# Optimization experiments

Hardware: AMD Instinct MI355X
Metric: run time of the kernel (lower is better)

Reference implementation:

```python
import jax, jax.numpy as jnp
import numpy as np

D = 768      # embedding_dim
M = 3072     # mlp_dim
G = 4        # num_expert_groups
E = 8        # experts_per_group
KG = 2       # k_groups
KE = 4       # k_experts
EPS = 1e-6   # gate weight threshold from the torch module


def setup_inputs() -> dict:
    key = jax.random.key(0)
    ks = jax.random.split(key, 9)
    x = jax.random.normal(ks[0], (1, 1024, D), dtype=jnp.float32)
    Wg = jax.random.normal(ks[1], (D, G), dtype=jnp.float32) * 0.02
    bg = jax.random.normal(ks[2], (G,), dtype=jnp.float32) * 0.01
    We = jax.random.normal(ks[3], (G, D, E), dtype=jnp.float32) * 0.02
    be = jax.random.normal(ks[4], (G, E), dtype=jnp.float32) * 0.01
    W1 = jax.random.normal(ks[5], (G, E, D, M), dtype=jnp.float32) * 0.02
    b1 = jax.random.normal(ks[6], (G, E, M), dtype=jnp.float32) * 0.01
    W2 = jax.random.normal(ks[7], (G, E, M, D), dtype=jnp.float32) * 0.02
    b2 = jax.random.normal(ks[8], (G, E, D), dtype=jnp.float32) * 0.01
    return {"x": x, "Wg": Wg, "bg": bg, "We": We, "be": be,
            "W1": W1, "b1": b1, "W2": W2, "b2": b2}


def _topk_gates(logits, k):
    # top-k logits -> softmax over the k entries, then zero out weights < 1e-6
    top, idx = jax.lax.top_k(logits, k)
    gates = jax.nn.softmax(top, axis=-1)
    gates = jnp.where(gates >= EPS, gates, jnp.zeros_like(gates))
    return gates, idx


def reference(x, Wg, bg, We, be, W1, b1, W2, b2):
    orig_shape = x.shape
    xf = x.reshape(-1, D)  # [N, D]

    # ---- level 1: group gating (eval mode: clean logits, no noise) ----
    glog = xf @ Wg + bg                      # [N, G]
    ggates, gidx = _topk_gates(glog, KG)     # [N, KG]
    gw = jnp.einsum('nk,nkg->ng', ggates,
                    jax.nn.one_hot(gidx, G, dtype=xf.dtype))  # dense [N, G]

    # ---- level 2: expert gating within each group ----
    # computed densely for all groups; unselected groups get zero group weight
    elog = jnp.einsum('nd,gde->nge', xf, We) + be  # [N, G, E]
    egates, eidx = _topk_gates(elog, KE)            # [N, G, KE]
    ew = jnp.einsum('ngk,ngke->nge', egates,
                    jax.nn.one_hot(eidx, E, dtype=xf.dtype))  # dense [N, G, E]

    combine = gw[:, :, None] * ew  # [N, G, E] combine weights

    # ---- expert MLPs (dense compute, combine-weighted sum) ----
    y = jnp.zeros_like(xf)
    for g in range(G):  # small fixed loop over expert groups
        h = jax.nn.gelu(jnp.einsum('nd,edm->enm', xf, W1[g]) + b1[g][:, None, :],
                        approximate=False)               # [E, N, M]
        o = jnp.einsum('enm,emd->end', h, W2[g]) + b2[g][:, None, :]  # [E, N, D]
        y = y + jnp.einsum('end,ne->nd', o, combine[:, g, :])
    return y.reshape(orig_shape)
```

## Files before the change

### kernel.cpp

```cpp
#include <hip/hip_runtime.h>
#include <hip/hip_bf16.h>
#include <math.h>

#define NTOK 1024
#define DDIM 768
#define MDIM 3072
#define GN 4
#define EN 8
#define NEXP 32
#define NPAIR 8192
#define EPSW 1e-6f
#define BYSPAN 3

typedef __attribute__((ext_vector_type(4))) float f32x4;
typedef __attribute__((ext_vector_type(4))) int   i32x4;
typedef __attribute__((ext_vector_type(4))) unsigned short u16x4;
typedef __attribute__((ext_vector_type(8))) __bf16 bf16x8;

__device__ __forceinline__ unsigned short f2bf(float f) {
  unsigned u = __builtin_bit_cast(unsigned, f);
  u += 0x7FFFu + ((u >> 16) & 1u);
  return (unsigned short)(u >> 16);
}

__global__ void init_kernel(int* __restrict__ p) { p[threadIdx.x] = 0; }

__global__ __launch_bounds__(256) void zero_y(float* __restrict__ y) {
  ((f32x4*)y)[blockIdx.x * 256 + threadIdx.x] = (f32x4){0.f, 0.f, 0.f, 0.f};
}

__global__ __launch_bounds__(256) void x2bf(const float* __restrict__ x,
                                            unsigned short* __restrict__ xb) {
  const int i = (blockIdx.x * 256 + threadIdx.x) * 16;
#pragma unroll
  for (int j = 0; j < 4; ++j) {
    const f32x4 v = *(const f32x4*)(x + i + j * 4);
    u16x4 p = { f2bf(v.x), f2bf(v.y), f2bf(v.z), f2bf(v.w) };
    *(u16x4*)(xb + i + j * 4) = p;
  }
}

__global__ __launch_bounds__(256) void gating_kernel(
    const float* __restrict__ x, const float* __restrict__ Wg,
    const float* __restrict__ bg, const float* __restrict__ We,
    const float* __restrict__ be, int* __restrict__ counts,
    int* __restrict__ pair_e, float* __restrict__ pair_w)
{
  __shared__ float xr[DDIM];
  __shared__ float logits[36];
  const int n = blockIdx.x;
  const int tid = threadIdx.x;
  const float* xp = x + (size_t)n * DDIM;
  for (int d = tid; d < DDIM; d += 256) xr[d] = xp[d];
  __syncthreads();

  const int w = tid >> 6, lane = tid & 63;
  for (int j = 0; j < 9; ++j) {
    const int o = w + 4 * j;
    float s = 0.f;
    if (o < 4) {
      for (int d = lane; d < DDIM; d += 64) s += xr[d] * Wg[d * GN + o];
    } else {
      const int g = (o - 4) >> 3, e = (o - 4) & 7;
      const float* wp = We + (size_t)g * DDIM * EN + e;
      for (int d = lane; d < DDIM; d += 64) s += xr[d] * wp[d * EN];
    }
    for (int off = 32; off; off >>= 1) s += __shfl_xor(s, off);
    if (lane == 0) logits[o] = s + ((o < 4) ? bg[o] : be[o - 4]);
  }
  __syncthreads();

  if (tid == 0) {
    float gl[4];
    for (int i = 0; i < 4; ++i) gl[i] = logits[i];
    int i0 = 0;
    for (int i = 1; i < 4; ++i) if (gl[i] > gl[i0]) i0 = i;
    int i1 = -1;
    for (int i = 0; i < 4; ++i) {
      if (i == i0) continue;
      if (i1 < 0 || gl[i] > gl[i1]) i1 = i;
    }
    const float m = gl[i0];
    const float e1 = expf(gl[i1] - m);
    const float s2 = 1.f + e1;
    float gv[2] = { 1.f / s2, e1 / s2 };
    int gi[2] = { i0, i1 };
    for (int r = 0; r < 2; ++r) if (gv[r] < EPSW) gv[r] = 0.f;

    for (int r = 0; r < 2; ++r) {
      const int g = gi[r];
      float el[8];
      for (int e = 0; e < 8; ++e) el[e] = logits[4 + g * 8 + e];
      int sel[4];
      for (int q = 0; q < 4; ++q) {
        int best = -1;
        for (int e = 0; e < 8; ++e) {
          bool used = false;
          for (int p = 0; p < q; ++p) if (sel[p] == e) used = true;
          if (used) continue;
          if (best < 0 || el[e] > el[best]) best = e;
        }
        sel[q] = best;
      }
      const float mm = el[sel[0]];
      float ex[4]; float ss = 0.f;
      for (int q = 0; q < 4; ++q) { ex[q] = expf(el[sel[q]] - mm); ss += ex[q]; }
      for (int q = 0; q < 4; ++q) {
        float ew = ex[q] / ss;
        if (ew < EPSW) ew = 0.f;
        const int gbl = g * 8 + sel[q];
        const int j = r * 4 + q;
        pair_e[n * 8 + j] = gbl;
        pair_w[n * 8 + j] = gv[r] * ew;
        atomicAdd(&counts[gbl], 1);
      }
    }
  }
}

__global__ void scan_kernel(const int* __restrict__ counts, int* __restrict__ offsets)
{
  if (threadIdx.x == 0) {
    int a = 0;
    for (int i = 0; i < NEXP; ++i) { offsets[i] = a; a += counts[i]; }
  }
}

__global__ __launch_bounds__(256) void scatter_kernel(
    const int* __restrict__ pair_e, const float* __restrict__ pair_w,
    const int* __restrict__ offsets, int* __restrict__ cursor,
    int* __restrict__ slot_tok, float* __restrict__ slot_w)
{
  const int idx = blockIdx.x * 256 + threadIdx.x;
  if (idx < NPAIR) {
    const int e = pair_e[idx];
    const int s = offsets[e] + atomicAdd(&cursor[e], 1);
    slot_tok[s] = idx >> 3;
    slot_w[s] = pair_w[idx];
  }
}

template<int K, int NLD, int EPI, int GATHER>
__global__ __launch_bounds__(256, 2) void moe_gemm_rs(
    const unsigned short* __restrict__ Abase, const float* __restrict__ W,
    const float* __restrict__ bias, const int* __restrict__ counts,
    const int* __restrict__ offsets, const float* __restrict__ slot_w,
    const int* __restrict__ slot_tok, unsigned short* __restrict__ Hout,
    float* __restrict__ Yout)
{
  constexpr int NT = K / 32;
  constexpr int BUFB = 16384;

  const int ge = blockIdx.z;
  const int cnt = counts[ge];
  const int nb = blockIdx.y;
  const int off = offsets[ge];
  const int tid = threadIdx.x;

  __shared__ __align__(16) unsigned char lds[2 * BUFB];

  const int am = tid >> 2, ac = tid & 3;
  const int asw0 = am * 64 + ((ac ^ ((am ^ (am >> 2)) & 3)) * 16);
  const int asw1 = asw0 + 4096;

  const int kq = tid >> 5, ln = tid & 31;
  const float* bp = W + (size_t)ge * K * NLD + (size_t)(kq * 4) * NLD + nb * 128 + ln;
  int bwr[4];
#pragma unroll
  for (int ii = 0; ii < 4; ++ii) {
    const int n = ln + 32 * ii;
    const int s = (n ^ (n >> 2)) & 3;
    bwr[ii] = 8192 + n * 64 + (((kq >> 1) ^ s) * 16) + ((kq & 1) * 8);
  }

  const int w = tid >> 6, lane = tid & 63;
  const int wr = (w >> 1) * 64, wc = (w & 1) * 64;
  const int l15 = lane & 15, l4 = lane >> 4;
  int aoff[4], boff[4];
#pragma unroll
  for (int mf = 0; mf < 4; ++mf) {
    const int m = wr + mf * 16 + l15;
    aoff[mf] = m * 64 + ((l4 ^ ((m ^ (m >> 2)) & 3)) * 16);
  }
#pragma unroll
  for (int nf = 0; nf < 4; ++nf) {
    const int n = wc + nf * 16 + l15;
    boff[nf] = 8192 + n * 64 + ((l4 ^ ((n ^ (n >> 2)) & 3)) * 16);
  }

  for (int by = blockIdx.x; by * 128 < cnt; by += BYSPAN) {
    int gr0 = by * 128 + am;      if (gr0 >= cnt) gr0 = cnt - 1;
    int gr1 = by * 128 + am + 64; if (gr1 >= cnt) gr1 = cnt - 1;
    const unsigned short* ap0;
    const unsigned short* ap1;
    if (GATHER) {
      ap0 = Abase + (size_t)slot_tok[off + gr0] * K + ac * 8;
      ap1 = Abase + (size_t)slot_tok[off + gr1] * K + ac * 8;
    } else {
      ap0 = Abase + (size_t)(off + gr0) * K + ac * 8;
      ap1 = Abase + (size_t)(off + gr1) * K + ac * 8;
    }

    f32x4 acc[4][4];
#pragma unroll
    for (int mf = 0; mf < 4; ++mf)
#pragma unroll
      for (int nf = 0; nf < 4; ++nf)
        acc[mf][nf] = (f32x4){0.f, 0.f, 0.f, 0.f};

    i32x4 aA0, aA1, aB0, aB1, aC0, aC1;
    float bA[16], bB[16], bC[16];

#define LOADA(T, R0, R1) { \
    R0 = *(const i32x4*)(ap0 + (T) * 32); \
    R1 = *(const i32x4*)(ap1 + (T) * 32); }
#define LOADB(T, BS) { _Pragma("unroll") \
    for (int ii = 0; ii < 4; ++ii) { _Pragma("unroll") \
      for (int jj = 0; jj < 4; ++jj) \
        BS[ii * 4 + jj] = bp[(size_t)((T) * 32 + jj) * NLD + 32 * ii]; } }
#define CVTW(R0, R1, BS, BASE) { \
    *(i32x4*)((BASE) + asw0) = R0; \
    *(i32x4*)((BASE) + asw1) = R1; \
    _Pragma("unroll") \
    for (int ii = 0; ii < 4; ++ii) { \
      u16x4 p = { f2bf(BS[ii*4+0]), f2bf(BS[ii*4+1]), f2bf(BS[ii*4+2]), f2bf(BS[ii*4+3]) }; \
      *(u16x4*)((BASE) + bwr[ii]) = p; } }
#define COMPUTE(BASE) { bf16x8 afr[4], bfr[4]; _Pragma("unroll") \
    for (int mf = 0; mf < 4; ++mf) \
      afr[mf] = __builtin_bit_cast(bf16x8, *(const i32x4*)((BASE) + aoff[mf])); \
    _Pragma("unroll") \
    for (int nf = 0; nf < 4; ++nf) \
      bfr[nf] = __builtin_bit_cast(bf16x8, *(const i32x4*)((BASE) + boff[nf])); \
    _Pragma("unroll") \
    for (int mf = 0; mf < 4; ++mf) { _Pragma("unroll") \
      for (int nf = 0; nf < 4; ++nf) \
        acc[mf][nf] = __builtin_amdgcn_mfma_f32_16x16x32_bf16( \
            afr[mf], bfr[nf], acc[mf][nf], 0, 0, 0); } }
#define STEP(T, C0, C1, CB, I0, I1, IB, BASE) { \
    if ((T) + 2 < NT) { LOADA((T) + 2, I0, I1); LOADB((T) + 2, IB); } \
    CVTW(C0, C1, CB, BASE); \
    asm volatile("s_waitcnt lgkmcnt(0)" ::: "memory"); \
    __builtin_amdgcn_s_barrier(); \
    COMPUTE(BASE); \
  }

    LOADA(0, aA0, aA1); LOADB(0, bA);
    LOADA(1, aB0, aB1); LOADB(1, bB);

    for (int t = 0; t < NT; t += 6) {
      STEP(t + 0, aA0, aA1, bA, aC0, aC1, bC, lds);
      STEP(t + 1, aB0, aB1, bB, aA0, aA1, bA, lds + BUFB);
      STEP(t + 2, aC0, aC1, bC, aB0, aB1, bB, lds);
      STEP(t + 3, aA0, aA1, bA, aC0, aC1, bC, lds + BUFB);
      STEP(t + 4, aB0, aB1, bB, aA0, aA1, bA, lds);
      STEP(t + 5, aC0, aC1, bC, aB0, aB1, bB, lds + BUFB);
    }
#undef LOADA
#undef LOADB
#undef CVTW
#undef COMPUTE
#undef STEP

#pragma unroll
    for (int mf = 0; mf < 4; ++mf) {
      const int rb = by * 128 + wr + mf * 16 + l4 * 4;
      if constexpr (EPI == 0) {
#pragma unroll
        for (int nf = 0; nf < 4; ++nf) {
          const int col = nb * 128 + wc + nf * 16 + l15;
          const float bv = bias[(size_t)ge * NLD + col];
#pragma unroll
          for (int j = 0; j < 4; ++j) {
            const int r = rb + j;
            if (r < cnt) {
              const float v = acc[mf][nf][j] + bv;
              const float gl = 0.5f * v * (1.f + erff(v * 0.70710678118654752f));
              Hout[(size_t)(off + r) * NLD + col] = f2bf(gl);
            }
          }
        }
      } else {
#pragma unroll
        for (int j = 0; j < 4; ++j) {
          const int r = rb + j;
          if (r < cnt) {
            const int slot = off + r;
            const float sw = slot_w[slot];
            const int tok = slot_tok[slot];
#pragma unroll
            for (int nf = 0; nf < 4; ++nf) {
              const int col = nb * 128 + wc + nf * 16 + l15;
              const float v = acc[mf][nf][j] + bias[(size_t)ge * NLD + col];
              atomicAdd(&Yout[(size_t)tok * DDIM + col], sw * v);
            }
          }
        }
      }
    }
  }
}

extern "C" void kernel_launch(void* const* d_in, const int* in_sizes, int n_in,
                              void* d_out, int out_size, void* d_ws, size_t ws_size,
                              hipStream_t stream)
{
  const float* x  = (const float*)d_in[0];
  const float* Wg = (const float*)d_in[1];
  const float* bg = (const float*)d_in[2];
  const float* We = (const float*)d_in[3];
  const float* be = (const float*)d_in[4];
  const float* W1 = (const float*)d_in[5];
  const float* b1 = (const float*)d_in[6];
  const float* W2 = (const float*)d_in[7];
  const float* b2 = (const float*)d_in[8];
  float* y = (float*)d_out;

  char* ws = (char*)d_ws;
  int*   counts   = (int*)(ws + 0);
  int*   offsets  = (int*)(ws + 256);
  int*   cursor   = (int*)(ws + 512);
  int*   pair_e   = (int*)(ws + 1024);
  float* pair_w   = (float*)(ws + 33792);
  int*   slot_tok = (int*)(ws + 66560);
  float* slot_w   = (float*)(ws + 99328);
  unsigned short* xb = (unsigned short*)(ws + 132096);
  unsigned short* H  = (unsigned short*)(ws + 12715008);

  init_kernel<<<1, 256, 0, stream>>>((int*)ws);
  zero_y<<<NTOK * DDIM / 1024, 256, 0, stream>>>(y);
  x2bf<<<NTOK * DDIM / 4096, 256, 0, stream>>>(x, xb);
  gating_kernel<<<NTOK, 256, 0, stream>>>(x, Wg, bg, We, be, counts, pair_e, pair_w);
  scan_kernel<<<1, 64, 0, stream>>>(counts, offsets);
  scatter_kernel<<<NPAIR / 256, 256, 0, stream>>>(pair_e, pair_w, offsets, cursor,
                                                  slot_tok, slot_w);

  moe_gemm_rs<DDIM, MDIM, 0, 1><<<dim3(BYSPAN, MDIM / 128, NEXP), 256, 0, stream>>>(
      xb, W1, b1, counts, offsets, nullptr, slot_tok, H, nullptr);
  moe_gemm_rs<MDIM, DDIM, 1, 0><<<dim3(BYSPAN, DDIM / 128, NEXP), 256, 0, stream>>>(
      H, W2, b2, counts, offsets, slot_w, slot_tok, nullptr, y);
}
```

Before: 493.8 us.

## Flatten expert row-block scheduling and split K for the down-projection GEMM

The scan kernel now also builds a flat list of (expert, row-block) work items. Both grouped GEMMs launch one block per work item instead of striding over row blocks inside each expert, which should even out load across experts with different token counts. The second GEMM also splits its 3072-long K dimension into four chunks. Each chunk atomically adds its partial result into the output, with the bias added only by the first chunk. Launch bounds are raised to 4 blocks per CU; this risks register spills, and the split adds four times as many output atomics.

```diff
diff --git a/kernel.cpp b/kernel.cpp
--- a/kernel.cpp
+++ b/kernel.cpp
@@ -10,7 +10,7 @@
 #define NEXP 32
 #define NPAIR 8192
 #define EPSW 1e-6f
-#define BYSPAN 3
+#define MAXRB 96
 
 typedef __attribute__((ext_vector_type(4))) float f32x4;
 typedef __attribute__((ext_vector_type(4))) int   i32x4;
@@ -118,11 +118,19 @@
   }
 }
 
-__global__ void scan_kernel(const int* __restrict__ counts, int* __restrict__ offsets)
+__global__ void scan_kernel(const int* __restrict__ counts, int* __restrict__ offsets,
+                            int* __restrict__ rb_ge, int* __restrict__ rb_by,
+                            int* __restrict__ nrb)
 {
   if (threadIdx.x == 0) {
-    int a = 0;
-    for (int i = 0; i < NEXP; ++i) { offsets[i] = a; a += counts[i]; }
+    int a = 0, n = 0;
+    for (int e = 0; e < NEXP; ++e) {
+      offsets[e] = a;
+      const int c = counts[e];
+      a += c;
+      for (int b = 0; b * 128 < c; ++b) { rb_ge[n] = e; rb_by[n] = b; ++n; }
+    }
+    *nrb = n;
   }
 }
 
@@ -140,21 +148,28 @@
   }
 }
 
-template<int K, int NLD, int EPI, int GATHER>
-__global__ __launch_bounds__(256, 2) void moe_gemm_rs(
+template<int K, int NLD, int EPI, int GATHER, int KS>
+__global__ __launch_bounds__(256, 4) void moe_gemm_fl(
     const unsigned short* __restrict__ Abase, const float* __restrict__ W,
     const float* __restrict__ bias, const int* __restrict__ counts,
     const int* __restrict__ offsets, const float* __restrict__ slot_w,
-    const int* __restrict__ slot_tok, unsigned short* __restrict__ Hout,
-    float* __restrict__ Yout)
-{
-  constexpr int NT = K / 32;
+    const int* __restrict__ slot_tok, const int* __restrict__ rb_ge,
+    const int* __restrict__ rb_by, const int* __restrict__ nrb,
+    unsigned short* __restrict__ Hout, float* __restrict__ Yout)
+{
+  constexpr int KC = K / KS;
+  constexpr int NT = KC / 32;
   constexpr int BUFB = 16384;
 
-  const int ge = blockIdx.z;
+  const int rb = blockIdx.x;
+  if (rb >= *nrb) return;
+  const int ge = rb_ge[rb];
+  const int by = rb_by[rb];
   const int cnt = counts[ge];
+  const int off = offsets[ge];
   const int nb = blockIdx.y;
-  const int off = offsets[ge];
+  const int ks = (KS > 1) ? blockIdx.z : 0;
+  const int kbase = ks * KC;
   const int tid = threadIdx.x;
 
   __shared__ __align__(16) unsigned char lds[2 * BUFB];
@@ -164,7 +179,8 @@
   const int asw1 = asw0 + 4096;
 
   const int kq = tid >> 5, ln = tid & 31;
-  const float* bp = W + (size_t)ge * K * NLD + (size_t)(kq * 4) * NLD + nb * 128 + ln;
+  const float* bp = W + (size_t)ge * K * NLD + (size_t)(kbase + kq * 4) * NLD
+                      + nb * 128 + ln;
   int bwr[4];
 #pragma unroll
   for (int ii = 0; ii < 4; ++ii) {
@@ -188,28 +204,27 @@
     boff[nf] = 8192 + n * 64 + ((l4 ^ ((n ^ (n >> 2)) & 3)) * 16);
   }
 
-  for (int by = blockIdx.x; by * 128 < cnt; by += BYSPAN) {
-    int gr0 = by * 128 + am;      if (gr0 >= cnt) gr0 = cnt - 1;
-    int gr1 = by * 128 + am + 64; if (gr1 >= cnt) gr1 = cnt - 1;
-    const unsigned short* ap0;
-    const unsigned short* ap1;
-    if (GATHER) {
-      ap0 = Abase + (size_t)slot_tok[off + gr0] * K + ac * 8;
-      ap1 = Abase + (size_t)slot_tok[off + gr1] * K + ac * 8;
-    } else {
-      ap0 = Abase + (size_t)(off + gr0) * K + ac * 8;
-      ap1 = Abase + (size_t)(off + gr1) * K + ac * 8;
-    }
-
-    f32x4 acc[4][4];
-#pragma unroll
-    for (int mf = 0; mf < 4; ++mf)
-#pragma unroll
-      for (int nf = 0; nf < 4; ++nf)
-        acc[mf][nf] = (f32x4){0.f, 0.f, 0.f, 0.f};
-
-    i32x4 aA0, aA1, aB0, aB1, aC0, aC1;
-    float bA[16], bB[16], bC[16];
+  int gr0 = by * 128 + am;      if (gr0 >= cnt) gr0 = cnt - 1;
+  int gr1 = by * 128 + am + 64; if (gr1 >= cnt) gr1 = cnt - 1;
+  const unsigned short* ap0;
+  const unsigned short* ap1;
+  if (GATHER) {
+    ap0 = Abase + (size_t)slot_tok[off + gr0] * K + kbase + ac * 8;
+    ap1 = Abase + (size_t)slot_tok[off + gr1] * K + kbase + ac * 8;
+  } else {
+    ap0 = Abase + (size_t)(off + gr0) * K + kbase + ac * 8;
+    ap1 = Abase + (size_t)(off + gr1) * K + kbase + ac * 8;
+  }
+
+  f32x4 acc[4][4];
+#pragma unroll
+  for (int mf = 0; mf < 4; ++mf)
+#pragma unroll
+    for (int nf = 0; nf < 4; ++nf)
+      acc[mf][nf] = (f32x4){0.f, 0.f, 0.f, 0.f};
+
+  i32x4 aA0, aA1, aB0, aB1, aC0, aC1;
+  float bA[16], bB[16], bC[16];
 
 #define LOADA(T, R0, R1) { \
     R0 = *(const i32x4*)(ap0 + (T) * 32); \
@@ -244,17 +259,17 @@
     COMPUTE(BASE); \
   }
 
-    LOADA(0, aA0, aA1); LOADB(0, bA);
-    LOADA(1, aB0, aB1); LOADB(1, bB);
-
-    for (int t = 0; t < NT; t += 6) {
-      STEP(t + 0, aA0, aA1, bA, aC0, aC1, bC, lds);
-      STEP(t + 1, aB0, aB1, bB, aA0, aA1, bA, lds + BUFB);
-      STEP(t + 2, aC0, aC1, bC, aB0, aB1, bB, lds);
-      STEP(t + 3, aA0, aA1, bA, aC0, aC1, bC, lds + BUFB);
-      STEP(t + 4, aB0, aB1, bB, aA0, aA1, bA, lds);
-      STEP(t + 5, aC0, aC1, bC, aB0, aB1, bB, lds + BUFB);
-    }
+  LOADA(0, aA0, aA1); LOADB(0, bA);
+  LOADA(1, aB0, aB1); LOADB(1, bB);
+
+  for (int t = 0; t < NT; t += 6) {
+    STEP(t + 0, aA0, aA1, bA, aC0, aC1, bC, lds);
+    STEP(t + 1, aB0, aB1, bB, aA0, aA1, bA, lds + BUFB);
+    STEP(t + 2, aC0, aC1, bC, aB0, aB1, bB, lds);
+    STEP(t + 3, aA0, aA1, bA, aC0, aC1, bC, lds + BUFB);
+    STEP(t + 4, aB0, aB1, bB, aA0, aA1, bA, lds);
+    STEP(t + 5, aC0, aC1, bC, aB0, aB1, bB, lds + BUFB);
+  }
 #undef LOADA
 #undef LOADB
 #undef CVTW
@@ -262,37 +277,36 @@
 #undef STEP
 
 #pragma unroll
-    for (int mf = 0; mf < 4; ++mf) {
-      const int rb = by * 128 + wr + mf * 16 + l4 * 4;
-      if constexpr (EPI == 0) {
-#pragma unroll
-        for (int nf = 0; nf < 4; ++nf) {
-          const int col = nb * 128 + wc + nf * 16 + l15;
-          const float bv = bias[(size_t)ge * NLD + col];
-#pragma unroll
-          for (int j = 0; j < 4; ++j) {
-            const int r = rb + j;
-            if (r < cnt) {
-              const float v = acc[mf][nf][j] + bv;
-              const float gl = 0.5f * v * (1.f + erff(v * 0.70710678118654752f));
-              Hout[(size_t)(off + r) * NLD + col] = f2bf(gl);
-            }
+  for (int mf = 0; mf < 4; ++mf) {
+    const int rb2 = by * 128 + wr + mf * 16 + l4 * 4;
+    if constexpr (EPI == 0) {
+#pragma unroll
+      for (int nf = 0; nf < 4; ++nf) {
+        const int col = nb * 128 + wc + nf * 16 + l15;
+        const float bv = bias[(size_t)ge * NLD + col];
+#pragma unroll
+        for (int j = 0; j < 4; ++j) {
+          const int r = rb2 + j;
+          if (r < cnt) {
+            const float v = acc[mf][nf][j] + bv;
+            const float gl = 0.5f * v * (1.f + erff(v * 0.70710678118654752f));
+            Hout[(size_t)(off + r) * NLD + col] = f2bf(gl);
           }
         }
-      } else {
-#pragma unroll
-        for (int j = 0; j < 4; ++j) {
-          const int r = rb + j;
-          if (r < cnt) {
-            const int slot = off + r;
-            const float sw = slot_w[slot];
-            const int tok = slot_tok[slot];
-#pragma unroll
-            for (int nf = 0; nf < 4; ++nf) {
-              const int col = nb * 128 + wc + nf * 16 + l15;
-              const float v = acc[mf][nf][j] + bias[(size_t)ge * NLD + col];
-              atomicAdd(&Yout[(size_t)tok * DDIM + col], sw * v);
-            }
+      }
+    } else {
+#pragma unroll
+      for (int j = 0; j < 4; ++j) {
+        const int r = rb2 + j;
+        if (r < cnt) {
+          const int slot = off + r;
+          const float sw = slot_w[slot];
+          const int tok = slot_tok[slot];
+#pragma unroll
+          for (int nf = 0; nf < 4; ++nf) {
+            const int col = nb * 128 + wc + nf * 16 + l15;
+            const float bv = (ks == 0) ? bias[(size_t)ge * NLD + col] : 0.f;
+            atomicAdd(&Yout[(size_t)tok * DDIM + col], sw * (acc[mf][nf][j] + bv));
           }
         }
       }
@@ -317,25 +331,28 @@
 
   char* ws = (char*)d_ws;
   int*   counts   = (int*)(ws + 0);
-  int*   offsets  = (int*)(ws + 256);
-  int*   cursor   = (int*)(ws + 512);
-  int*   pair_e   = (int*)(ws + 1024);
-  float* pair_w   = (float*)(ws + 33792);
-  int*   slot_tok = (int*)(ws + 66560);
-  float* slot_w   = (float*)(ws + 99328);
-  unsigned short* xb = (unsigned short*)(ws + 132096);
+  int*   offsets  = (int*)(ws + 128);
+  int*   cursor   = (int*)(ws + 256);
+  int*   nrb      = (int*)(ws + 384);
+  int*   rb_ge    = (int*)(ws + 512);
+  int*   rb_by    = (int*)(ws + 896);
+  int*   pair_e   = (int*)(ws + 2048);
+  float* pair_w   = (float*)(ws + 34816);
+  int*   slot_tok = (int*)(ws + 67584);
+  float* slot_w   = (float*)(ws + 100352);
+  unsigned short* xb = (unsigned short*)(ws + 135168);
   unsigned short* H  = (unsigned short*)(ws + 12715008);
 
   init_kernel<<<1, 256, 0, stream>>>((int*)ws);
   zero_y<<<NTOK * DDIM / 1024, 256, 0, stream>>>(y);
   x2bf<<<NTOK * DDIM / 4096, 256, 0, stream>>>(x, xb);
   gating_kernel<<<NTOK, 256, 0, stream>>>(x, Wg, bg, We, be, counts, pair_e, pair_w);
-  scan_kernel<<<1, 64, 0, stream>>>(counts, offsets);
+  scan_kernel<<<1, 64, 0, stream>>>(counts, offsets, rb_ge, rb_by, nrb);
   scatter_kernel<<<NPAIR / 256, 256, 0, stream>>>(pair_e, pair_w, offsets, cursor,
                                                   slot_tok, slot_w);
 
-  moe_gemm_rs<DDIM, MDIM, 0, 1><<<dim3(BYSPAN, MDIM / 128, NEXP), 256, 0, stream>>>(
-      xb, W1, b1, counts, offsets, nullptr, slot_tok, H, nullptr);
-  moe_gemm_rs<MDIM, DDIM, 1, 0><<<dim3(BYSPAN, DDIM / 128, NEXP), 256, 0, stream>>>(
-      H, W2, b2, counts, offsets, slot_w, slot_tok, nullptr, y);
-}
+  moe_gemm_fl<DDIM, MDIM, 0, 1, 1><<<dim3(MAXRB, MDIM / 128, 1), 256, 0, stream>>>(
+      xb, W1, b1, counts, offsets, nullptr, slot_tok, rb_ge, rb_by, nrb, H, nullptr);
+  moe_gemm_fl<MDIM, DDIM, 1, 0, 4><<<dim3(MAXRB, DDIM / 128, 4), 256, 0, stream>>>(
+      H, W2, b2, counts, offsets, slot_w, slot_tok, rb_ge, rb_by, nrb, nullptr, y);
+}
```

Measured after the change: 1.671 ms. 3.38x slower.
